# Performance work log

Measured on AMD Instinct MI355X. Metric: run time of the kernel, lower is better.

Reference implementation:

```python
import jax, jax.numpy as jnp
import numpy as np

NEG_SLOPE = 0.01  # F.leaky_relu default
DROP_P = 0.5      # F.dropout(p=0.5, training=True by default in this code)


def _lrelu(x):
    return jnp.where(x >= 0, x, NEG_SLOPE * x)


def _hconv(Xi, X, Ht, Hs, edge_w, theta, w_trans, bias):
    # Faithful to Ht.T @ diag(edge_w) @ Hs @ X @ theta + Xi @ w_trans + bias,
    # with diag(edge_w) fused as a per-row scale of the [E, out] intermediate.
    msg = (Hs @ X) @ theta                 # [E, out]
    agg = Ht.T @ (edge_w[:, None] * msg)   # [N, out]
    return _lrelu(agg + Xi @ w_trans + bias)


def setup_inputs() -> dict:
    key = jax.random.key(0)
    ks = jax.random.split(key, 14)
    N, E, F0, H = 8192, 4096, 128, 128
    f32 = jnp.float32
    return {
        "xi": jax.random.normal(ks[0], (N, F0), f32),
        "x": jax.random.normal(ks[1], (N, F0), f32),
        "Ht": jax.random.uniform(ks[2], (E, N), f32),
        "Hs": jax.random.uniform(ks[3], (E, N), f32),
        "state": jax.random.normal(ks[4], (N, 1), f32),
        # conv0 params (std=0.01 init as in torch code)
        "w_trans0": 0.01 * jax.random.normal(ks[5], (F0, H), f32),
        "theta0": 0.01 * jax.random.normal(ks[6], (F0, H), f32),
        "edge_w0": jnp.ones((E,), f32),
        "bias0": 0.01 * jax.random.normal(ks[7], (H,), f32),
        # conv1 params
        "w_trans1": 0.01 * jax.random.normal(ks[8], (H, H), f32),
        "theta1": 0.01 * jax.random.normal(ks[9], (H, H), f32),
        "edge_w1": jnp.ones((E,), f32),
        "bias1": 0.01 * jax.random.normal(ks[10], (H,), f32),
        # fc: Linear(H+1, 1)
        "fc_w": 0.01 * jax.random.normal(ks[11], (H + 1, 1), f32),
        "fc_b": 0.01 * jax.random.normal(ks[12], (1,), f32),
    }


def reference(xi, x, Ht, Hs, state,
              w_trans0, theta0, edge_w0, bias0,
              w_trans1, theta1, edge_w1, bias1,
              fc_w, fc_b):
    X1 = _hconv(xi, x, Ht, Hs, edge_w0, theta0, w_trans0, bias0)  # [N, H]
    # F.dropout(p=0.5) is active (training=True default); fixed mask for determinism
    keep = jax.random.bernoulli(jax.random.key(42), 1.0 - DROP_P, X1.shape)
    X1 = jnp.where(keep, X1 / (1.0 - DROP_P), 0.0)
    X2 = _hconv(xi, X1, Ht, Hs, edge_w1, theta1, w_trans1, bias1)  # [N, H]
    X = _lrelu(X2)  # second leaky_relu, as in DQN.forward
    Xc = jnp.concatenate([X, state], axis=1)  # [N, H+1]
    return Xc @ fc_w + fc_b  # [N, 1]
```

## Files before the change

### kernel.cpp

```cpp
#include <hip/hip_runtime.h>
#include <hip/hip_bf16.h>
#include <stdint.h>


typedef short short8 __attribute__((ext_vector_type(8)));
typedef float f32x4 __attribute__((ext_vector_type(4)));

static constexpr int N = 8192, E = 4096, F = 128;
static constexpr int SA = 8, SB = 4;

__device__ __forceinline__ unsigned rotl32(unsigned x, int r) {
  return (x << r) | (x >> (32 - r));
}

__device__ __forceinline__ uint2 threefry2x32(unsigned k0, unsigned k1,
                                              unsigned x0, unsigned x1) {
  unsigned ks[3] = {k0, k1, k0 ^ k1 ^ 0x1BD11BDAu};
  x0 += ks[0];
  x1 += ks[1];
  const int R0[4] = {13, 15, 26, 6};
  const int R1[4] = {17, 29, 16, 24};
#pragma unroll
  for (int i = 0; i < 5; ++i) {
#pragma unroll
    for (int j = 0; j < 4; ++j) {
      const int r = (i % 2 == 0) ? R0[j] : R1[j];
      x0 += x1;
      x1 = rotl32(x1, r);
      x1 ^= x0;
    }
    x0 += ks[(i + 1) % 3];
    x1 += ks[(i + 2) % 3] + (unsigned)(i + 1);
  }
  return make_uint2(x0, x1);
}

__device__ __forceinline__ float drop_scale(unsigned idx) {
  const uint2 o = threefry2x32(0u, 42u, 0u, idx);
  return ((o.x ^ o.y) & 0x80000000u) ? 0.0f : 2.0f;
}

__device__ __forceinline__ float lrelu(float v) {
  return v >= 0.0f ? v : 0.01f * v;
}

__device__ __forceinline__ unsigned rne1(float a) {
  unsigned ua = __builtin_bit_cast(unsigned, a);
  ua += 0x7fffu + ((ua >> 16) & 1u);
  return ua >> 16;
}
__device__ __forceinline__ float bf16_val(unsigned u16) {
  return __builtin_bit_cast(float, u16 << 16);
}
__device__ __forceinline__ unsigned pk_bf16(float a, float b) {
  return rne1(a) | (rne1(b) << 16);
}
__device__ __forceinline__ void split2(float a, float b, unsigned& hi,
                                       unsigned& lo) {
  const unsigned ha = rne1(a), hb = rne1(b);
  const float ra = a - bf16_val(ha), rb = b - bf16_val(hb);
  hi = ha | (hb << 16);
  lo = rne1(ra) | (rne1(rb) << 16);
}

template <bool TRANSA>
__global__ __launch_bounds__(256) void big_gemm(
    const float* __restrict__ A, const float* __restrict__ Bt,
    float* __restrict__ P, int M, int K, int lda, int kchunk) {
  __shared__ __align__(16) short As[128 * 40];
  __shared__ __align__(16) short Bh[128 * 40];
  __shared__ __align__(16) short Bl[128 * 40];

  const int tid = threadIdx.x;
  const int lane = tid & 63;
  const int w = tid >> 6;
  const int wm = (w & 1) << 6;
  const int wn = (w >> 1) << 6;
  const int l15 = lane & 15;
  const int koff = (lane >> 4) << 3;

  const int r0 = blockIdx.x * 128;
  const int s = blockIdx.y;
  const int kbeg = s * kchunk;
  const int kend = kbeg + kchunk;

  f32x4 acc[4][4];
#pragma unroll
  for (int i = 0; i < 4; ++i)
#pragma unroll
    for (int j = 0; j < 4; ++j) acc[i][j] = (f32x4){0.f, 0.f, 0.f, 0.f};

  for (int k0 = kbeg; k0 < kend; k0 += 32) {
    if (!TRANSA) {
#pragma unroll
      for (int i = 0; i < 4; ++i) {
        const int f = i * 256 + tid;
        const int m = f >> 3;
        const int kq = f & 7;
        const float4 v =
            *(const float4*)(A + (size_t)(r0 + m) * lda + k0 + 4 * kq);
        uint2 u = {pk_bf16(v.x, v.y), pk_bf16(v.z, v.w)};
        *(uint2*)&As[m * 40 + 4 * kq] = u;
      }
    } else {
#pragma unroll
      for (int i = 0; i < 2; ++i) {
        const int f = i * 256 + tid;
        const int m = f & 127;
        const int eo = f >> 7;
        float vv[8];
#pragma unroll
        for (int r = 0; r < 8; ++r)
          vv[r] = A[(size_t)(k0 + 8 * eo + r) * lda + (r0 + m)];
        uint4 u = {pk_bf16(vv[0], vv[1]), pk_bf16(vv[2], vv[3]),
                   pk_bf16(vv[4], vv[5]), pk_bf16(vv[6], vv[7])};
        *(uint4*)&As[m * 40 + 8 * eo] = u;
      }
    }
#pragma unroll
    for (int i = 0; i < 4; ++i) {
      const int q = i * 256 + tid;
      const int c = q >> 3;
      const int kq = q & 7;
      const float4 v = *(const float4*)(Bt + (size_t)c * K + k0 + 4 * kq);
      uint2 uh, ul;
      split2(v.x, v.y, uh.x, ul.x);
      split2(v.z, v.w, uh.y, ul.y);
      *(uint2*)&Bh[c * 40 + 4 * kq] = uh;
      *(uint2*)&Bl[c * 40 + 4 * kq] = ul;
    }
    __syncthreads();

    short8 af[4], bh[4], bl[4];
#pragma unroll
    for (int i = 0; i < 4; ++i)
      af[i] = *(const short8*)&As[(wm + 16 * i + l15) * 40 + koff];
#pragma unroll
    for (int j = 0; j < 4; ++j) {
      bh[j] = *(const short8*)&Bh[(wn + 16 * j + l15) * 40 + koff];
      bl[j] = *(const short8*)&Bl[(wn + 16 * j + l15) * 40 + koff];
    }
#pragma unroll
    for (int i = 0; i < 4; ++i)
#pragma unroll
      for (int j = 0; j < 4; ++j) {
        acc[i][j] = __builtin_amdgcn_mfma_f32_16x16x32_bf16(af[i], bl[j],
                                                            acc[i][j], 0, 0, 0);
        acc[i][j] = __builtin_amdgcn_mfma_f32_16x16x32_bf16(af[i], bh[j],
                                                            acc[i][j], 0, 0, 0);
      }
    __syncthreads();
  }

  const int rquad = (lane >> 4) << 2;
#pragma unroll
  for (int i = 0; i < 4; ++i)
#pragma unroll
    for (int j = 0; j < 4; ++j)
#pragma unroll
      for (int r = 0; r < 4; ++r) {
        const int row = r0 + wm + 16 * i + rquad + r;
        const int col = wn + 16 * j + l15;
        P[((size_t)s * M + row) * 128 + col] = acc[i][j][r];
      }
}

template <bool WA>
__global__ __launch_bounds__(256) void small_gemm(
    const float* __restrict__ src, const float* __restrict__ W,
    float* __restrict__ out) {
  __shared__ __align__(16) short WTh[128 * 40], WTl[128 * 40];
  __shared__ __align__(16) short Xh[64 * 40], Xl[64 * 40];

  const int tid = threadIdx.x;
  const int lane = tid & 63;
  const int w = tid >> 6;
  const int l15 = lane & 15;
  const int n0 = blockIdx.x * 64;

  constexpr int TI = WA ? 4 : 2;
  constexpr int TJ = WA ? 2 : 4;
  const int wm = (w & 1) * (WA ? 64 : 32);
  const int wn = (w >> 1) * (WA ? 32 : 64);

  f32x4 acc[TI][TJ];
#pragma unroll
  for (int i = 0; i < TI; ++i)
#pragma unroll
    for (int j = 0; j < TJ; ++j) acc[i][j] = (f32x4){0.f, 0.f, 0.f, 0.f};

  for (int k0 = 0; k0 < 128; k0 += 32) {
#pragma unroll
    for (int i = 0; i < 2; ++i) {
      const int f = i * 256 + tid;
      const int c = f & 127;
      const int eo = f >> 7;
      uint4 uh, ul;
      unsigned* ph = (unsigned*)&uh;
      unsigned* pl = (unsigned*)&ul;
#pragma unroll
      for (int r = 0; r < 4; ++r) {
        const float a = W[(size_t)(k0 + 8 * eo + 2 * r) * 128 + c];
        const float b = W[(size_t)(k0 + 8 * eo + 2 * r + 1) * 128 + c];
        split2(a, b, ph[r], pl[r]);
      }
      *(uint4*)&WTh[c * 40 + 8 * eo] = uh;
      *(uint4*)&WTl[c * 40 + 8 * eo] = ul;
    }
#pragma unroll
    for (int i = 0; i < 2; ++i) {
      const int q = i * 256 + tid;
      const int n = q >> 3;
      const int kq = q & 7;
      const float4 v = *(const float4*)(src + (size_t)(n0 + n) * 128 + k0 + 4 * kq);
      uint2 uh, ul;
      split2(v.x, v.y, uh.x, ul.x);
      split2(v.z, v.w, uh.y, ul.y);
      *(uint2*)&Xh[n * 40 + 4 * kq] = uh;
      *(uint2*)&Xl[n * 40 + 4 * kq] = ul;
    }
    __syncthreads();

    const int koff = (lane >> 4) << 3;
    short8 ah[TI], al[TI], bh[TJ], bl[TJ];
#pragma unroll
    for (int i = 0; i < TI; ++i) {
      const int m = wm + 16 * i + l15;
      ah[i] = WA ? *(const short8*)&WTh[m * 40 + koff]
                 : *(const short8*)&Xh[m * 40 + koff];
      al[i] = WA ? *(const short8*)&WTl[m * 40 + koff]
                 : *(const short8*)&Xl[m * 40 + koff];
    }
#pragma unroll
    for (int j = 0; j < TJ; ++j) {
      const int c = wn + 16 * j + l15;
      bh[j] = WA ? *(const short8*)&Xh[c * 40 + koff]
                 : *(const short8*)&WTh[c * 40 + koff];
      bl[j] = WA ? *(const short8*)&Xl[c * 40 + koff]
                 : *(const short8*)&WTl[c * 40 + koff];
    }
#pragma unroll
    for (int i = 0; i < TI; ++i)
#pragma unroll
      for (int j = 0; j < TJ; ++j) {
        acc[i][j] = __builtin_amdgcn_mfma_f32_16x16x32_bf16(al[i], bh[j],
                                                            acc[i][j], 0, 0, 0);
        acc[i][j] = __builtin_amdgcn_mfma_f32_16x16x32_bf16(ah[i], bl[j],
                                                            acc[i][j], 0, 0, 0);
        acc[i][j] = __builtin_amdgcn_mfma_f32_16x16x32_bf16(ah[i], bh[j],
                                                            acc[i][j], 0, 0, 0);
      }
    __syncthreads();
  }

  const int rquad = (lane >> 4) << 2;
#pragma unroll
  for (int i = 0; i < TI; ++i)
#pragma unroll
    for (int j = 0; j < TJ; ++j)
#pragma unroll
      for (int r = 0; r < 4; ++r) {
        const int row = wm + 16 * i + rquad + r;
        const int col = wn + 16 * j + l15;
        if (WA)
          out[(size_t)row * N + n0 + col] = acc[i][j][r];
        else
          out[(size_t)(n0 + row) * 128 + col] = acc[i][j][r];
      }
}

__global__ __launch_bounds__(256) void reduce_A(const float* __restrict__ P,
                                                const float* __restrict__ ew,
                                                float* __restrict__ Mt) {
  __shared__ float Lt[32 * 132];
  const int tid = threadIdx.x;
  const int e0 = blockIdx.x * 32;
#pragma unroll
  for (int i = 0; i < 4; ++i) {
    const int f = i * 256 + tid;
    const int el = f >> 5;
    const int cq = f & 31;
    float4 a = {0.f, 0.f, 0.f, 0.f};
#pragma unroll
    for (int s = 0; s < SA; ++s) {
      const float4 v =
          *(const float4*)(P + ((size_t)s * E + e0 + el) * 128 + 4 * cq);
      a.x += v.x; a.y += v.y; a.z += v.z; a.w += v.w;
    }
    const float sc = ew[e0 + el];
    a.x *= sc; a.y *= sc; a.z *= sc; a.w *= sc;
    *(float4*)&Lt[el * 132 + 4 * cq] = a;
  }
  __syncthreads();
#pragma unroll
  for (int i = 0; i < 4; ++i) {
    const int g = i * 256 + tid;
    const int c = g >> 3;
    const int eq = g & 7;
    float4 o;
    o.x = Lt[(4 * eq + 0) * 132 + c];
    o.y = Lt[(4 * eq + 1) * 132 + c];
    o.z = Lt[(4 * eq + 2) * 132 + c];
    o.w = Lt[(4 * eq + 3) * 132 + c];
    *(float4*)&Mt[(size_t)c * E + e0 + 4 * eq] = o;
  }
}

__global__ __launch_bounds__(256) void reduce_B1(const float* __restrict__ P,
                                                 const float* __restrict__ Badd,
                                                 const float* __restrict__ bias,
                                                 float* __restrict__ X1) {
  const int q = blockIdx.x * 256 + threadIdx.x;
  const int n = q >> 5;
  const int cq = q & 31;
  float4 a = {0.f, 0.f, 0.f, 0.f};
#pragma unroll
  for (int s = 0; s < SB; ++s) {
    const float4 v = *(const float4*)(P + ((size_t)s * N + n) * 128 + 4 * cq);
    a.x += v.x; a.y += v.y; a.z += v.z; a.w += v.w;
  }
  const float4 b = *(const float4*)(Badd + (size_t)n * 128 + 4 * cq);
  const float4 bi = *(const float4*)(bias + 4 * cq);
  const unsigned fb = (unsigned)(n * 128 + 4 * cq);
  float4 o;
  o.x = lrelu(a.x + b.x + bi.x) * drop_scale(fb + 0u);
  o.y = lrelu(a.y + b.y + bi.y) * drop_scale(fb + 1u);
  o.z = lrelu(a.z + b.z + bi.z) * drop_scale(fb + 2u);
  o.w = lrelu(a.w + b.w + bi.w) * drop_scale(fb + 3u);
  *(float4*)&X1[(size_t)n * 128 + 4 * cq] = o;
}

__global__ __launch_bounds__(256) void reduce_B2(
    const float* __restrict__ P, const float* __restrict__ Badd,
    const float* __restrict__ bias, const float* __restrict__ fcw,
    const float* __restrict__ state, const float* __restrict__ fcb,
    float* __restrict__ out) {
  __shared__ float part[4];
  const int tid = threadIdx.x;
  const int nn = tid >> 7;
  const int c = tid & 127;
  const int n = blockIdx.x * 2 + nn;
  float v = 0.f;
#pragma unroll
  for (int s = 0; s < SB; ++s) v += P[((size_t)s * N + n) * 128 + c];
  v += Badd[(size_t)n * 128 + c] + bias[c];
  float p = lrelu(lrelu(v)) * fcw[c];
#pragma unroll
  for (int m = 32; m >= 1; m >>= 1) p += __shfl_xor(p, m, 64);
  if ((tid & 63) == 0) part[tid >> 6] = p;
  __syncthreads();
  if (tid < 2)
    out[blockIdx.x * 2 + tid] = part[2 * tid] + part[2 * tid + 1] +
                                state[blockIdx.x * 2 + tid] * fcw[128] + fcb[0];
}

extern "C" void kernel_launch(void* const* d_in, const int* in_sizes, int n_in,
                              void* d_out, int out_size, void* d_ws,
                              size_t ws_size, hipStream_t stream) {
  (void)in_sizes; (void)n_in; (void)out_size; (void)ws_size;

  const float* xi = (const float*)d_in[0];
  const float* x = (const float*)d_in[1];
  const float* Ht = (const float*)d_in[2];
  const float* Hs = (const float*)d_in[3];
  const float* state = (const float*)d_in[4];
  const float* wt0 = (const float*)d_in[5];
  const float* th0 = (const float*)d_in[6];
  const float* ew0 = (const float*)d_in[7];
  const float* bi0 = (const float*)d_in[8];
  const float* wt1 = (const float*)d_in[9];
  const float* th1 = (const float*)d_in[10];
  const float* ew1 = (const float*)d_in[11];
  const float* bi1 = (const float*)d_in[12];
  const float* fcw = (const float*)d_in[13];
  const float* fcb = (const float*)d_in[14];
  float* out = (float*)d_out;

  float* ws = (float*)d_ws;
  float* P = ws;
  float* Tt = P + (size_t)4194304;
  float* Badd = Tt + (size_t)N * F;
  float* Mt = Badd + (size_t)N * F;
  float* X1 = Mt + (size_t)E * F;

  const dim3 blk(256);

  small_gemm<true><<<N / 64, blk, 0, stream>>>(x, th0, Tt);
  small_gemm<false><<<N / 64, blk, 0, stream>>>(xi, wt0, Badd);
  big_gemm<false><<<dim3(E / 128, SA), blk, 0, stream>>>(Hs, Tt, P, E, N, N,
                                                         N / SA);
  reduce_A<<<E / 32, blk, 0, stream>>>(P, ew0, Mt);
  big_gemm<true><<<dim3(N / 128, SB), blk, 0, stream>>>(Ht, Mt, P, N, E, N,
                                                        E / SB);
  reduce_B1<<<N * F / 4 / 256, blk, 0, stream>>>(P, Badd, bi0, X1);

  small_gemm<true><<<N / 64, blk, 0, stream>>>(X1, th1, Tt);
  small_gemm<false><<<N / 64, blk, 0, stream>>>(xi, wt1, Badd);
  big_gemm<false><<<dim3(E / 128, SA), blk, 0, stream>>>(Hs, Tt, P, E, N, N,
                                                         N / SA);
  reduce_A<<<E / 32, blk, 0, stream>>>(P, ew1, Mt);
  big_gemm<true><<<dim3(N / 128, SB), blk, 0, stream>>>(Ht, Mt, P, N, E, N,
                                                        E / SB);
  reduce_B2<<<N / 2, blk, 0, stream>>>(P, Badd, bi1, fcw, state, fcb, out);
}
```

Measured before the change: 524.0 us.

## Double-buffer big GEMM with 512 threads, double split-K, fuse small GEMMs

The big split-K GEMM now prefetches the next K tile from global memory into registers while MFMAs run on the current LDS buffer, using two LDS buffers and eight waves per block. Split-K factors are doubled to put more blocks on the device. The two small projection GEMMs are merged into one launch with the bias folded into Badd. reduce_A is retuned to a smaller tile. In exchange, more LDS per block and larger partial-sum buffers raise the reduction traffic.

```diff
diff --git a/kernel.cpp b/kernel.cpp
--- a/kernel.cpp
+++ b/kernel.cpp
@@ -1,5 +1,4 @@
 #include <hip/hip_runtime.h>
-#include <hip/hip_bf16.h>
 #include <stdint.h>
 
 
@@ -7,7 +6,7 @@
 typedef float f32x4 __attribute__((ext_vector_type(4)));
 
 static constexpr int N = 8192, E = 4096, F = 128;
-static constexpr int SA = 8, SB = 4;
+static constexpr int SA = 16, SB = 8;
 
 __device__ __forceinline__ unsigned rotl32(unsigned x, int r) {
   return (x << r) | (x >> (32 - r));
@@ -64,97 +63,123 @@
 }
 
 template <bool TRANSA>
-__global__ __launch_bounds__(256) void big_gemm(
+__global__ __launch_bounds__(512, 4) void big_gemm(
     const float* __restrict__ A, const float* __restrict__ Bt,
     float* __restrict__ P, int M, int K, int lda, int kchunk) {
-  __shared__ __align__(16) short As[128 * 40];
-  __shared__ __align__(16) short Bh[128 * 40];
-  __shared__ __align__(16) short Bl[128 * 40];
+  __shared__ __align__(16) short As[2][128 * 40];
+  __shared__ __align__(16) short Bh[2][128 * 40];
+  __shared__ __align__(16) short Bl[2][128 * 40];
 
   const int tid = threadIdx.x;
   const int lane = tid & 63;
   const int w = tid >> 6;
-  const int wm = (w & 1) << 6;
-  const int wn = (w >> 1) << 6;
+  const int wm = (w & 3) << 5;
+  const int wn = (w >> 2) << 6;
   const int l15 = lane & 15;
   const int koff = (lane >> 4) << 3;
 
   const int r0 = blockIdx.x * 128;
   const int s = blockIdx.y;
   const int kbeg = s * kchunk;
-  const int kend = kbeg + kchunk;
-
-  f32x4 acc[4][4];
-#pragma unroll
-  for (int i = 0; i < 4; ++i)
-#pragma unroll
-    for (int j = 0; j < 4; ++j) acc[i][j] = (f32x4){0.f, 0.f, 0.f, 0.f};
-
-  for (int k0 = kbeg; k0 < kend; k0 += 32) {
+  const int nt = kchunk >> 5;
+
+  float4 ra[2], rb[2];
+
+  auto loadg = [&](int kt) {
     if (!TRANSA) {
 #pragma unroll
-      for (int i = 0; i < 4; ++i) {
-        const int f = i * 256 + tid;
+      for (int i = 0; i < 2; ++i) {
+        const int f = i * 512 + tid;
         const int m = f >> 3;
         const int kq = f & 7;
-        const float4 v =
-            *(const float4*)(A + (size_t)(r0 + m) * lda + k0 + 4 * kq);
-        uint2 u = {pk_bf16(v.x, v.y), pk_bf16(v.z, v.w)};
-        *(uint2*)&As[m * 40 + 4 * kq] = u;
+        ra[i] = *(const float4*)(A + (size_t)(r0 + m) * lda + kt + 4 * kq);
       }
     } else {
-#pragma unroll
-      for (int i = 0; i < 2; ++i) {
-        const int f = i * 256 + tid;
-        const int m = f & 127;
-        const int eo = f >> 7;
-        float vv[8];
-#pragma unroll
-        for (int r = 0; r < 8; ++r)
-          vv[r] = A[(size_t)(k0 + 8 * eo + r) * lda + (r0 + m)];
-        uint4 u = {pk_bf16(vv[0], vv[1]), pk_bf16(vv[2], vv[3]),
-                   pk_bf16(vv[4], vv[5]), pk_bf16(vv[6], vv[7])};
-        *(uint4*)&As[m * 40 + 8 * eo] = u;
-      }
-    }
-#pragma unroll
-    for (int i = 0; i < 4; ++i) {
-      const int q = i * 256 + tid;
+      const int m = tid & 127;
+      const int eo = tid >> 7;
+      float* v = (float*)ra;
+#pragma unroll
+      for (int r = 0; r < 8; ++r)
+        v[r] = A[(size_t)(kt + 8 * eo + r) * lda + r0 + m];
+    }
+#pragma unroll
+    for (int i = 0; i < 2; ++i) {
+      const int q = i * 512 + tid;
       const int c = q >> 3;
       const int kq = q & 7;
-      const float4 v = *(const float4*)(Bt + (size_t)c * K + k0 + 4 * kq);
+      rb[i] = *(const float4*)(Bt + (size_t)c * K + kt + 4 * kq);
+    }
+  };
+
+  auto store_lds = [&](int buf) {
+    if (!TRANSA) {
+#pragma unroll
+      for (int i = 0; i < 2; ++i) {
+        const int f = i * 512 + tid;
+        const int m = f >> 3;
+        const int kq = f & 7;
+        uint2 u = {pk_bf16(ra[i].x, ra[i].y), pk_bf16(ra[i].z, ra[i].w)};
+        *(uint2*)&As[buf][m * 40 + 4 * kq] = u;
+      }
+    } else {
+      const int m = tid & 127;
+      const int eo = tid >> 7;
+      const float* v = (const float*)ra;
+      uint4 u = {pk_bf16(v[0], v[1]), pk_bf16(v[2], v[3]),
+                 pk_bf16(v[4], v[5]), pk_bf16(v[6], v[7])};
+      *(uint4*)&As[buf][m * 40 + 8 * eo] = u;
+    }
+#pragma unroll
+    for (int i = 0; i < 2; ++i) {
+      const int q = i * 512 + tid;
+      const int c = q >> 3;
+      const int kq = q & 7;
       uint2 uh, ul;
-      split2(v.x, v.y, uh.x, ul.x);
-      split2(v.z, v.w, uh.y, ul.y);
-      *(uint2*)&Bh[c * 40 + 4 * kq] = uh;
-      *(uint2*)&Bl[c * 40 + 4 * kq] = ul;
-    }
+      split2(rb[i].x, rb[i].y, uh.x, ul.x);
+      split2(rb[i].z, rb[i].w, uh.y, ul.y);
+      *(uint2*)&Bh[buf][c * 40 + 4 * kq] = uh;
+      *(uint2*)&Bl[buf][c * 40 + 4 * kq] = ul;
+    }
+  };
+
+  f32x4 acc[2][4];
+#pragma unroll
+  for (int i = 0; i < 2; ++i)
+#pragma unroll
+    for (int j = 0; j < 4; ++j) acc[i][j] = (f32x4){0.f, 0.f, 0.f, 0.f};
+
+  loadg(kbeg);
+  store_lds(0);
+  int cur = 0;
+  for (int t = 0; t < nt; ++t) {
     __syncthreads();
-
-    short8 af[4], bh[4], bl[4];
-#pragma unroll
-    for (int i = 0; i < 4; ++i)
-      af[i] = *(const short8*)&As[(wm + 16 * i + l15) * 40 + koff];
+    if (t + 1 < nt) loadg(kbeg + 32 * (t + 1));
+
+    short8 af[2], bhf[4], blf[4];
+#pragma unroll
+    for (int i = 0; i < 2; ++i)
+      af[i] = *(const short8*)&As[cur][(wm + 16 * i + l15) * 40 + koff];
 #pragma unroll
     for (int j = 0; j < 4; ++j) {
-      bh[j] = *(const short8*)&Bh[(wn + 16 * j + l15) * 40 + koff];
-      bl[j] = *(const short8*)&Bl[(wn + 16 * j + l15) * 40 + koff];
-    }
-#pragma unroll
-    for (int i = 0; i < 4; ++i)
+      bhf[j] = *(const short8*)&Bh[cur][(wn + 16 * j + l15) * 40 + koff];
+      blf[j] = *(const short8*)&Bl[cur][(wn + 16 * j + l15) * 40 + koff];
+    }
+#pragma unroll
+    for (int i = 0; i < 2; ++i)
 #pragma unroll
       for (int j = 0; j < 4; ++j) {
-        acc[i][j] = __builtin_amdgcn_mfma_f32_16x16x32_bf16(af[i], bl[j],
+        acc[i][j] = __builtin_amdgcn_mfma_f32_16x16x32_bf16(af[i], blf[j],
                                                             acc[i][j], 0, 0, 0);
-        acc[i][j] = __builtin_amdgcn_mfma_f32_16x16x32_bf16(af[i], bh[j],
+        acc[i][j] = __builtin_amdgcn_mfma_f32_16x16x32_bf16(af[i], bhf[j],
                                                             acc[i][j], 0, 0, 0);
       }
-    __syncthreads();
+    if (t + 1 < nt) store_lds(cur ^ 1);
+    cur ^= 1;
   }
 
   const int rquad = (lane >> 4) << 2;
 #pragma unroll
-  for (int i = 0; i < 4; ++i)
+  for (int i = 0; i < 2; ++i)
 #pragma unroll
     for (int j = 0; j < 4; ++j)
 #pragma unroll
@@ -166,20 +191,15 @@
 }
 
 template <bool WA>
-__global__ __launch_bounds__(256) void small_gemm(
+__device__ __forceinline__ void small_core(
     const float* __restrict__ src, const float* __restrict__ W,
-    float* __restrict__ out) {
-  __shared__ __align__(16) short WTh[128 * 40], WTl[128 * 40];
-  __shared__ __align__(16) short Xh[64 * 40], Xl[64 * 40];
-
-  const int tid = threadIdx.x;
+    const float* __restrict__ bias, float* __restrict__ out, short* WTh,
+    short* WTl, short* Xh, short* Xl, int n0, int tid) {
+  constexpr int TI = WA ? 4 : 2;
+  constexpr int TJ = WA ? 2 : 4;
   const int lane = tid & 63;
   const int w = tid >> 6;
   const int l15 = lane & 15;
-  const int n0 = blockIdx.x * 64;
-
-  constexpr int TI = WA ? 4 : 2;
-  constexpr int TJ = WA ? 2 : 4;
   const int wm = (w & 1) * (WA ? 64 : 32);
   const int wn = (w >> 1) * (WA ? 32 : 64);
 
@@ -212,7 +232,8 @@
       const int q = i * 256 + tid;
       const int n = q >> 3;
       const int kq = q & 7;
-      const float4 v = *(const float4*)(src + (size_t)(n0 + n) * 128 + k0 + 4 * kq);
+      const float4 v =
+          *(const float4*)(src + (size_t)(n0 + n) * 128 + k0 + 4 * kq);
       uint2 uh, ul;
       split2(v.x, v.y, uh.x, ul.x);
       split2(v.z, v.w, uh.y, ul.y);
@@ -262,21 +283,37 @@
       for (int r = 0; r < 4; ++r) {
         const int row = wm + 16 * i + rquad + r;
         const int col = wn + 16 * j + l15;
-        if (WA)
+        if constexpr (WA)
           out[(size_t)row * N + n0 + col] = acc[i][j][r];
         else
-          out[(size_t)(n0 + row) * 128 + col] = acc[i][j][r];
-      }
+          out[(size_t)(n0 + row) * 128 + col] = acc[i][j][r] + bias[col];
+      }
+}
+
+__global__ __launch_bounds__(256) void small_fused(
+    const float* __restrict__ srcT, const float* __restrict__ Wth,
+    const float* __restrict__ srcB, const float* __restrict__ Wwt,
+    const float* __restrict__ bias, float* __restrict__ Tt,
+    float* __restrict__ Badd) {
+  __shared__ __align__(16) short WTh[128 * 40], WTl[128 * 40];
+  __shared__ __align__(16) short Xh[64 * 40], Xl[64 * 40];
+  const int n0 = blockIdx.x * 64;
+  if (blockIdx.y == 0)
+    small_core<true>(srcT, Wth, nullptr, Tt, WTh, WTl, Xh, Xl, n0,
+                     threadIdx.x);
+  else
+    small_core<false>(srcB, Wwt, bias, Badd, WTh, WTl, Xh, Xl, n0,
+                      threadIdx.x);
 }
 
 __global__ __launch_bounds__(256) void reduce_A(const float* __restrict__ P,
                                                 const float* __restrict__ ew,
                                                 float* __restrict__ Mt) {
-  __shared__ float Lt[32 * 132];
+  __shared__ float Lt[16 * 132];
   const int tid = threadIdx.x;
-  const int e0 = blockIdx.x * 32;
-#pragma unroll
-  for (int i = 0; i < 4; ++i) {
+  const int e0 = blockIdx.x * 16;
+#pragma unroll
+  for (int i = 0; i < 2; ++i) {
     const int f = i * 256 + tid;
     const int el = f >> 5;
     const int cq = f & 31;
@@ -293,10 +330,10 @@
   }
   __syncthreads();
 #pragma unroll
-  for (int i = 0; i < 4; ++i) {
+  for (int i = 0; i < 2; ++i) {
     const int g = i * 256 + tid;
-    const int c = g >> 3;
-    const int eq = g & 7;
+    const int c = g >> 2;
+    const int eq = g & 3;
     float4 o;
     o.x = Lt[(4 * eq + 0) * 132 + c];
     o.y = Lt[(4 * eq + 1) * 132 + c];
@@ -308,7 +345,6 @@
 
 __global__ __launch_bounds__(256) void reduce_B1(const float* __restrict__ P,
                                                  const float* __restrict__ Badd,
-                                                 const float* __restrict__ bias,
                                                  float* __restrict__ X1) {
   const int q = blockIdx.x * 256 + threadIdx.x;
   const int n = q >> 5;
@@ -320,21 +356,19 @@
     a.x += v.x; a.y += v.y; a.z += v.z; a.w += v.w;
   }
   const float4 b = *(const float4*)(Badd + (size_t)n * 128 + 4 * cq);
-  const float4 bi = *(const float4*)(bias + 4 * cq);
   const unsigned fb = (unsigned)(n * 128 + 4 * cq);
   float4 o;
-  o.x = lrelu(a.x + b.x + bi.x) * drop_scale(fb + 0u);
-  o.y = lrelu(a.y + b.y + bi.y) * drop_scale(fb + 1u);
-  o.z = lrelu(a.z + b.z + bi.z) * drop_scale(fb + 2u);
-  o.w = lrelu(a.w + b.w + bi.w) * drop_scale(fb + 3u);
+  o.x = lrelu(a.x + b.x) * drop_scale(fb + 0u);
+  o.y = lrelu(a.y + b.y) * drop_scale(fb + 1u);
+  o.z = lrelu(a.z + b.z) * drop_scale(fb + 2u);
+  o.w = lrelu(a.w + b.w) * drop_scale(fb + 3u);
   *(float4*)&X1[(size_t)n * 128 + 4 * cq] = o;
 }
 
 __global__ __launch_bounds__(256) void reduce_B2(
     const float* __restrict__ P, const float* __restrict__ Badd,
-    const float* __restrict__ bias, const float* __restrict__ fcw,
-    const float* __restrict__ state, const float* __restrict__ fcb,
-    float* __restrict__ out) {
+    const float* __restrict__ fcw, const float* __restrict__ state,
+    const float* __restrict__ fcb, float* __restrict__ out) {
   __shared__ float part[4];
   const int tid = threadIdx.x;
   const int nn = tid >> 7;
@@ -343,7 +377,7 @@
   float v = 0.f;
 #pragma unroll
   for (int s = 0; s < SB; ++s) v += P[((size_t)s * N + n) * 128 + c];
-  v += Badd[(size_t)n * 128 + c] + bias[c];
+  v += Badd[(size_t)n * 128 + c];
   float p = lrelu(lrelu(v)) * fcw[c];
 #pragma unroll
   for (int m = 32; m >= 1; m >>= 1) p += __shfl_xor(p, m, 64);
@@ -378,28 +412,26 @@
 
   float* ws = (float*)d_ws;
   float* P = ws;
-  float* Tt = P + (size_t)4194304;
-  float* Badd = Tt + (size_t)N * F;
+  float* Tt = P + (size_t)SA * E * F;
+  float* Badd = Tt + (size_t)F * N;
   float* Mt = Badd + (size_t)N * F;
-  float* X1 = Mt + (size_t)E * F;
-
-  const dim3 blk(256);
-
-  small_gemm<true><<<N / 64, blk, 0, stream>>>(x, th0, Tt);
-  small_gemm<false><<<N / 64, blk, 0, stream>>>(xi, wt0, Badd);
-  big_gemm<false><<<dim3(E / 128, SA), blk, 0, stream>>>(Hs, Tt, P, E, N, N,
+  float* X1 = Mt + (size_t)F * E;
+
+  small_fused<<<dim3(N / 64, 2), 256, 0, stream>>>(x, th0, xi, wt0, bi0, Tt,
+                                                   Badd);
+  big_gemm<false><<<dim3(E / 128, SA), 512, 0, stream>>>(Hs, Tt, P, E, N, N,
                                                          N / SA);
-  reduce_A<<<E / 32, blk, 0, stream>>>(P, ew0, Mt);
-  big_gemm<true><<<dim3(N / 128, SB), blk, 0, stream>>>(Ht, Mt, P, N, E, N,
+  reduce_A<<<E / 16, 256, 0, stream>>>(P, ew0, Mt);
+  big_gemm<true><<<dim3(N / 128, SB), 512, 0, stream>>>(Ht, Mt, P, N, E, N,
                                                         E / SB);
-  reduce_B1<<<N * F / 4 / 256, blk, 0, stream>>>(P, Badd, bi0, X1);
-
-  small_gemm<true><<<N / 64, blk, 0, stream>>>(X1, th1, Tt);
-  small_gemm<false><<<N / 64, blk, 0, stream>>>(xi, wt1, Badd);
-  big_gemm<false><<<dim3(E / 128, SA), blk, 0, stream>>>(Hs, Tt, P, E, N, N,
+  reduce_B1<<<N * F / 4 / 256, 256, 0, stream>>>(P, Badd, X1);
+
+  small_fused<<<dim3(N / 64, 2), 256, 0, stream>>>(X1, th1, xi, wt1, bi1, Tt,
+                                                   Badd);
+  big_gemm<false><<<dim3(E / 128, SA), 512, 0, stream>>>(Hs, Tt, P, E, N, N,
                                                          N / SA);
-  reduce_A<<<E / 32, blk, 0, stream>>>(P, ew1, Mt);
-  big_gemm<true><<<dim3(N / 128, SB), blk, 0, stream>>>(Ht, Mt, P, N, E, N,
+  reduce_A<<<E / 16, 256, 0, stream>>>(P, ew1, Mt);
+  big_gemm<true><<<dim3(N / 128, SB), 512, 0, stream>>>(Ht, Mt, P, N, E, N,
                                                         E / SB);
-  reduce_B2<<<N / 2, blk, 0, stream>>>(P, Badd, bi1, fcw, state, fcb, out);
-}
+  reduce_B2<<<N / 2, 256, 0, stream>>>(P, Badd, fcw, state, fcb, out);
+}
```

Measured after the change: 448.0 us. 14.5% less time.
